# Performance work log

Measured on AMD Instinct MI355X. Metric: run time of the kernel, lower is better.

The kernel has to match this reference:

```python
import jax, jax.numpy as jnp
import numpy as np

MARGIN = 0.1  # GatingFunction margin_threshold default


def _gating(x, gW1, gb1, gW2, gb2):
    # two-layer MLP + softmax over experts: [B, E]
    h = jax.nn.relu(x @ gW1 + gb1)
    probs = jax.nn.softmax(h @ gW2 + gb2, axis=1)

    # sequential per-sample running-assignment masking (training + mask_enabled path)
    def step(rta, s):
        rta1 = rta + s
        mask = rta1 > rta1.mean() + MARGIN
        rta2 = jnp.where(mask.any(), rta1 - s, rta1)  # subtract back only if any masked
        mod = jnp.where(mask, 0.0, s)
        norm = mod.sum()
        mod = mod / jnp.where(norm == 0, 1.0, norm)
        return rta2 + mod, mod

    rta0 = jnp.zeros((gW2.shape[1],), probs.dtype)  # running_total_assignment buffer
    _, gate = jax.lax.scan(step, rta0, probs)
    # torch code writes detached modified samples into modified_x -> no grad through gate
    return jax.lax.stop_gradient(gate)


def reference(x_expert, gW1, gb1, gW2, gb2, eW1, eb1, eW2, eb2):
    gate = _gating(x_expert, gW1, gb1, gW2, gb2)          # [B, E]
    # all experts run densely: [B, E, H] -> [B, E, O]
    h = jax.nn.relu(jnp.einsum('bi,eih->beh', x_expert, eW1) + eb1)
    expert_out = jnp.einsum('beh,eho->beo', h, eW2) + eb2
    g = gate[:, :, None]                                   # [B, E, 1]
    # fallback if every gate value is zero (torch's all-zero check)
    g = jnp.where(jnp.all(g == 0), jnp.ones_like(g) / g.shape[1], g)
    output = jnp.sum(g * expert_out, axis=1)               # [B, O]
    return output, g


def setup_inputs() -> dict:
    B, IN, HID, OUT, E = 4096, 1024, 4096, 1024, 8
    key = jax.random.key(0)
    ks = jax.random.split(key, 9)
    s = 0.02
    return {
        'x_expert': jax.random.normal(ks[0], (B, IN), jnp.float32),
        'gW1': jax.random.normal(ks[1], (IN, HID), jnp.float32) * s,
        'gb1': jnp.zeros((HID,), jnp.float32),
        'gW2': jax.random.normal(ks[2], (HID, E), jnp.float32) * s,
        'gb2': jnp.zeros((E,), jnp.float32),
        'eW1': jax.random.normal(ks[3], (E, IN, HID), jnp.float32) * s,
        'eb1': jnp.zeros((E, HID), jnp.float32),
        'eW2': jax.random.normal(ks[4], (E, HID, OUT), jnp.float32) * s,
        'eb2': jnp.zeros((E, OUT), jnp.float32),
    }
```

## Files before the change

kernel.cpp:

```cpp
#include <hip/hip_runtime.h>
#include <stdint.h>

using f32x4  = __attribute__((ext_vector_type(4))) float;
using bf16x8 = __attribute__((ext_vector_type(8))) __bf16;

static __device__ __forceinline__ unsigned short f2bf(float f) {
  union { float f; unsigned int u; } v; v.f = f;
  return (unsigned short)((v.u + 0x7fffu + ((v.u >> 16) & 1u)) >> 16);
}

static __device__ __forceinline__ void gload_lds16(const void* g, void* l) {
  __builtin_amdgcn_global_load_lds((const __attribute__((address_space(1))) void*)g,
                                   (__attribute__((address_space(3))) void*)l,
                                   16, 0, 0);
}

static __device__ __forceinline__ int swz(int row) { return (row & 3) ^ ((row >> 2) & 3); }

template <int CTRL>
static __device__ __forceinline__ float dppadd(float x) {
  int xi = __builtin_bit_cast(int, x);
  int yi = __builtin_amdgcn_update_dpp(0, xi, CTRL, 0xF, 0xF, true);
  return x + __builtin_bit_cast(float, yi);
}
static __device__ __forceinline__ float redsum8(float x) {
  float t = dppadd<0xB1>(x);
  t = dppadd<0x4E>(t);
  t = dppadd<0x124>(t);
  return t;
}

__global__ __launch_bounds__(256) void k_cvt_bf16(const float* __restrict__ in,
                                                  unsigned short* __restrict__ out) {
  int i = blockIdx.x * 256 + threadIdx.x;
  float4 v = ((const float4*)in)[i];
  ushort4 o;
  o.x = f2bf(v.x); o.y = f2bf(v.y); o.z = f2bf(v.z); o.w = f2bf(v.w);
  ((ushort4*)out)[i] = o;
}

__global__ __launch_bounds__(256) void k_transpose_cvt(const float* __restrict__ in,
                                                       unsigned short* __restrict__ out,
                                                       int R, int C) {
  __shared__ float tile[32][33];
  int e = blockIdx.z;
  const float* ip = in + (size_t)e * R * C;
  unsigned short* op = out + (size_t)e * R * C;
  int c0 = blockIdx.x * 32, r0 = blockIdx.y * 32;
  int tx = threadIdx.x, ty = threadIdx.y;
  #pragma unroll
  for (int i = ty; i < 32; i += 8)
    tile[i][tx] = ip[(size_t)(r0 + i) * C + c0 + tx];
  __syncthreads();
  #pragma unroll
  for (int i = ty; i < 32; i += 8)
    op[(size_t)(c0 + i) * R + r0 + tx] = f2bf(tile[tx][i]);
}

__global__ __launch_bounds__(256) void k_gemm_f32_relu(const float* __restrict__ A,
                                                       const float* __restrict__ Bm,
                                                       const float* __restrict__ bias,
                                                       float* __restrict__ C) {
  const int K = 1024, N = 4096;
  __shared__ float As[16][128];
  __shared__ float Bs[16][128];
  int n0 = blockIdx.x * 128, m0 = blockIdx.y * 128;
  int t = threadIdx.x;
  int tm = t >> 4, tn = t & 15;
  float acc[8][8];
  #pragma unroll
  for (int i = 0; i < 8; ++i)
    #pragma unroll
    for (int j = 0; j < 8; ++j) acc[i][j] = 0.f;

  for (int k0 = 0; k0 < K; k0 += 16) {
    __syncthreads();
    #pragma unroll
    for (int cc = 0; cc < 2; ++cc) {
      int c = t + cc * 256;
      int m = c >> 2, kq = c & 3;
      float4 v = *(const float4*)&A[(size_t)(m0 + m) * K + k0 + kq * 4];
      As[kq * 4 + 0][m] = v.x; As[kq * 4 + 1][m] = v.y;
      As[kq * 4 + 2][m] = v.z; As[kq * 4 + 3][m] = v.w;
    }
    #pragma unroll
    for (int cc = 0; cc < 2; ++cc) {
      int c = t + cc * 256;
      int kr = c >> 5, nq = c & 31;
      *(float4*)&Bs[kr][nq * 4] = *(const float4*)&Bm[(size_t)(k0 + kr) * N + n0 + nq * 4];
    }
    __syncthreads();
    #pragma unroll
    for (int kk = 0; kk < 16; ++kk) {
      float a[8], b[8];
      *(float4*)&a[0] = *(const float4*)&As[kk][tm * 8];
      *(float4*)&a[4] = *(const float4*)&As[kk][tm * 8 + 4];
      *(float4*)&b[0] = *(const float4*)&Bs[kk][tn * 8];
      *(float4*)&b[4] = *(const float4*)&Bs[kk][tn * 8 + 4];
      #pragma unroll
      for (int i = 0; i < 8; ++i)
        #pragma unroll
        for (int j = 0; j < 8; ++j) acc[i][j] = fmaf(a[i], b[j], acc[i][j]);
    }
  }
  float bb[8];
  #pragma unroll
  for (int j = 0; j < 8; ++j) bb[j] = bias[n0 + tn * 8 + j];
  #pragma unroll
  for (int i = 0; i < 8; ++i) {
    int m = m0 + tm * 8 + i;
    float* crow = C + (size_t)m * N + n0 + tn * 8;
    float4 v0, v1;
    v0.x = fmaxf(acc[i][0] + bb[0], 0.f); v0.y = fmaxf(acc[i][1] + bb[1], 0.f);
    v0.z = fmaxf(acc[i][2] + bb[2], 0.f); v0.w = fmaxf(acc[i][3] + bb[3], 0.f);
    v1.x = fmaxf(acc[i][4] + bb[4], 0.f); v1.y = fmaxf(acc[i][5] + bb[5], 0.f);
    v1.z = fmaxf(acc[i][6] + bb[6], 0.f); v1.w = fmaxf(acc[i][7] + bb[7], 0.f);
    *(float4*)crow = v0; *(float4*)(crow + 4) = v1;
  }
}

__global__ __launch_bounds__(256) void k_gate2_softmax(const float* __restrict__ Hg,
                                                       const float* __restrict__ gW2,
                                                       const float* __restrict__ gb2,
                                                       float* __restrict__ probs) {
  __shared__ float red[4][8];
  int b = blockIdx.x, t = threadIdx.x;
  const float* hrow = Hg + (size_t)b * 4096;
  float acc[8];
  #pragma unroll
  for (int e = 0; e < 8; ++e) acc[e] = 0.f;
  #pragma unroll
  for (int i = 0; i < 4; ++i) {
    int kk = t + i * 256;
    float4 h = ((const float4*)hrow)[kk];
    const float* wr = gW2 + (size_t)kk * 32;
    #pragma unroll
    for (int j = 0; j < 4; ++j) {
      float hv = (&h.x)[j];
      #pragma unroll
      for (int e = 0; e < 8; ++e) acc[e] = fmaf(hv, wr[j * 8 + e], acc[e]);
    }
  }
  #pragma unroll
  for (int e = 0; e < 8; ++e) {
    float v = acc[e];
    for (int off = 32; off > 0; off >>= 1) v += __shfl_down(v, off);
    acc[e] = v;
  }
  int lane = t & 63, w = t >> 6;
  if (lane == 0) {
    #pragma unroll
    for (int e = 0; e < 8; ++e) red[w][e] = acc[e];
  }
  __syncthreads();
  if (t == 0) {
    float l[8], mx = -1e30f;
    #pragma unroll
    for (int e = 0; e < 8; ++e) {
      l[e] = red[0][e] + red[1][e] + red[2][e] + red[3][e] + gb2[e];
      mx = fmaxf(mx, l[e]);
    }
    float sum = 0.f;
    #pragma unroll
    for (int e = 0; e < 8; ++e) { l[e] = expf(l[e] - mx); sum += l[e]; }
    float inv = 1.f / sum;
    #pragma unroll
    for (int e = 0; e < 8; ++e) probs[b * 8 + e] = l[e] * inv;
  }
}

__global__ __launch_bounds__(256) void k_egemm1_scan(const unsigned short* __restrict__ Xb,
                                                     const unsigned short* __restrict__ W1T,
                                                     const float* __restrict__ eb1,
                                                     const float* __restrict__ probs,
                                                     float* __restrict__ gateOut,
                                                     unsigned short* __restrict__ Hs) {
  __shared__ __align__(16) char smem[33024];
  int bid = blockIdx.x;
  int t = threadIdx.x;

  if (bid == 0) {
    float* P  = (float*)smem;
    float* G  = P + 4096;
    int*  flg = (int*)(G + 4096);
    int e = t & 7;
    float rta = 0.f, maxn = 0.f;
    for (int ch = 0; ch < 8; ++ch) {
      __syncthreads();
      #pragma unroll
      for (int i = 0; i < 4; ++i)
        ((float4*)P)[t + i * 256] = ((const float4*)(probs + ch * 4096))[t + i * 256];
      __syncthreads();
      if (t < 64) {
        float s_cur = P[e];
        for (int r = 0; r < 512; ++r) {
          float s_nxt = P[(((r + 1) & 511) << 3) + e];
          float a = rta + s_cur;
          float sum = redsum8(a);
          float thr = fmaf(sum, 0.125f, 0.1f);
          bool msk = a > thr;
          unsigned long long bal = __ballot(msk);
          float d = msk ? 0.f : s_cur;
          float norm = redsum8(d);
          float inv = (norm == 0.f) ? 1.f : (1.f / norm);
          float g = d * inv;
          float base = (bal != 0ull) ? (a - s_cur) : a;
          rta = base + g;
          maxn = fmaxf(maxn, norm);
          if (t < 8) G[(r << 3) + e] = g;
          s_cur = s_nxt;
        }
      }
      __syncthreads();
      #pragma unroll
      for (int i = 0; i < 4; ++i)
        ((float4*)(gateOut + ch * 4096))[t + i * 256] = ((const float4*)G)[t + i * 256];
    }
    if (t == 0) *flg = (maxn > 0.f) ? 1 : 0;
    __syncthreads();
    if (*flg == 0) {
      for (int i = t; i < 32768; i += 256) gateOut[i] = 0.125f;
    }
    return;
  }

  char* Asm = smem;
  char* Bsm = smem + 8192;
  int b = bid - 1;
  int e = b >> 10;
  int rest = b & 1023;
  int m0 = (rest >> 5) << 7, n0 = (rest & 31) << 7;
  int lane = t & 63, w = t >> 6;
  int wm = w >> 1, wn = w & 1;
  const unsigned short* Ab = Xb;
  const unsigned short* Bb = W1T + ((size_t)e << 22);
  f32x4 acc[4][4];
  #pragma unroll
  for (int mi = 0; mi < 4; ++mi)
    #pragma unroll
    for (int ni = 0; ni < 4; ++ni) acc[mi][ni] = (f32x4){0.f, 0.f, 0.f, 0.f};

  for (int kt = 0; kt < 1024; kt += 32) {
    __syncthreads();
    {
      int p = (w << 6) + lane;
      int row = p >> 2, h = (p & 3) ^ swz(row);
      int p2 = p + 256;
      int row2 = p2 >> 2, h2 = (p2 & 3) ^ swz(row2);
      char* la = Asm + (w << 10);
      char* lb = Bsm + (w << 10);
      gload_lds16(Ab + (size_t)(m0 + row) * 1024 + kt + h * 8, la);
      gload_lds16(Ab + (size_t)(m0 + row2) * 1024 + kt + h2 * 8, la + 4096);
      gload_lds16(Bb + (size_t)(n0 + row) * 1024 + kt + h * 8, lb);
      gload_lds16(Bb + (size_t)(n0 + row2) * 1024 + kt + h2 * 8, lb + 4096);
    }
    __syncthreads();
    bf16x8 af[4], bfr[4];
    #pragma unroll
    for (int mi = 0; mi < 4; ++mi) {
      int ra = (wm << 6) + (mi << 4) + (lane & 15);
      int hh = (lane >> 4) ^ swz(ra);
      af[mi] = *(const bf16x8*)(Asm + ra * 64 + hh * 16);
    }
    #pragma unroll
    for (int ni = 0; ni < 4; ++ni) {
      int rb = (wn << 6) + (ni << 4) + (lane & 15);
      int hh = (lane >> 4) ^ swz(rb);
      bfr[ni] = *(const bf16x8*)(Bsm + rb * 64 + hh * 16);
    }
    #pragma unroll
    for (int mi = 0; mi < 4; ++mi)
      #pragma unroll
      for (int ni = 0; ni < 4; ++ni)
        acc[mi][ni] = __builtin_amdgcn_mfma_f32_16x16x32_bf16(af[mi], bfr[ni], acc[mi][ni], 0, 0, 0);
  }
  const float* b1e = eb1 + (e << 12);
  unsigned short* Ho = Hs + ((size_t)e << 24);
  int col = lane & 15, quad = lane >> 4;
  float bn[4];
  #pragma unroll
  for (int ni = 0; ni < 4; ++ni) bn[ni] = b1e[n0 + (wn << 6) + (ni << 4) + col];
  #pragma unroll
  for (int mi = 0; mi < 4; ++mi) {
    #pragma unroll
    for (int r = 0; r < 4; ++r) {
      int m = m0 + (wm << 6) + (mi << 4) + (quad << 2) + r;
      unsigned short* orow = Ho + (size_t)m * 4096 + n0 + (wn << 6) + col;
      #pragma unroll
      for (int ni = 0; ni < 4; ++ni) {
        float v = fmaxf(acc[mi][ni][r] + bn[ni], 0.f);
        orow[ni << 4] = f2bf(v);
      }
    }
  }
}

__global__ __launch_bounds__(256) void k_egemm2(const unsigned short* __restrict__ Hs,
                                                const unsigned short* __restrict__ W2T,
                                                float* __restrict__ partLo,
                                                float* __restrict__ partHi) {
  __shared__ __align__(16) char Asm[8192];
  __shared__ __align__(16) char Bsm[8192];
  int bid = blockIdx.x;
  int n0 = (bid >> 8) << 7;
  int rem = bid & 255;
  int m0 = (rem >> 3) << 7;
  int e = rem & 7;
  int t = threadIdx.x, lane = t & 63, w = t >> 6;
  int wm = w >> 1, wn = w & 1;
  const unsigned short* Ab = Hs + ((size_t)e << 24);
  const unsigned short* Bb = W2T + ((size_t)e << 22);
  f32x4 acc[4][4];
  #pragma unroll
  for (int mi = 0; mi < 4; ++mi)
    #pragma unroll
    for (int ni = 0; ni < 4; ++ni) acc[mi][ni] = (f32x4){0.f, 0.f, 0.f, 0.f};

  for (int kt = 0; kt < 4096; kt += 32) {
    __syncthreads();
    {
      int p = (w << 6) + lane;
      int row = p >> 2, h = (p & 3) ^ swz(row);
      int p2 = p + 256;
      int row2 = p2 >> 2, h2 = (p2 & 3) ^ swz(row2);
      char* la = Asm + (w << 10);
      char* lb = Bsm + (w << 10);
      gload_lds16(Ab + (size_t)(m0 + row) * 4096 + kt + h * 8, la);
      gload_lds16(Ab + (size_t)(m0 + row2) * 4096 + kt + h2 * 8, la + 4096);
      gload_lds16(Bb + (size_t)(n0 + row) * 4096 + kt + h * 8, lb);
      gload_lds16(Bb + (size_t)(n0 + row2) * 4096 + kt + h2 * 8, lb + 4096);
    }
    __syncthreads();
    bf16x8 af[4], bfr[4];
    #pragma unroll
    for (int mi = 0; mi < 4; ++mi) {
      int ra = (wm << 6) + (mi << 4) + (lane & 15);
      int hh = (lane >> 4) ^ swz(ra);
      af[mi] = *(const bf16x8*)(Asm + ra * 64 + hh * 16);
    }
    #pragma unroll
    for (int ni = 0; ni < 4; ++ni) {
      int rb = (wn << 6) + (ni << 4) + (lane & 15);
      int hh = (lane >> 4) ^ swz(rb);
      bfr[ni] = *(const bf16x8*)(Bsm + rb * 64 + hh * 16);
    }
    #pragma unroll
    for (int mi = 0; mi < 4; ++mi)
      #pragma unroll
      for (int ni = 0; ni < 4; ++ni)
        acc[mi][ni] = __builtin_amdgcn_mfma_f32_16x16x32_bf16(af[mi], bfr[ni], acc[mi][ni], 0, 0, 0);
  }
  float* Pe = (e < 4 ? partLo + ((size_t)e << 22) : partHi + ((size_t)(e - 4) << 22));
  int col = lane & 15, quad = lane >> 4;
  #pragma unroll
  for (int mi = 0; mi < 4; ++mi) {
    #pragma unroll
    for (int r = 0; r < 4; ++r) {
      int m = m0 + (wm << 6) + (mi << 4) + (quad << 2) + r;
      float* orow = Pe + (size_t)m * 1024 + n0 + (wn << 6) + col;
      #pragma unroll
      for (int ni = 0; ni < 4; ++ni) orow[ni << 4] = acc[mi][ni][r];
    }
  }
}

__global__ __launch_bounds__(256) void k_reduce(const float* __restrict__ partLo,
                                                const float* __restrict__ partHi,
                                                const float* __restrict__ eb2,
                                                const float* __restrict__ gate,
                                                float* __restrict__ Out) {
  int idx = blockIdx.x * 256 + threadIdx.x;
  int m = idx >> 8, n4 = idx & 255;
  float4 g0 = *(const float4*)(gate + (m << 3));
  float4 g1 = *(const float4*)(gate + (m << 3) + 4);
  float ga[8] = {g0.x, g0.y, g0.z, g0.w, g1.x, g1.y, g1.z, g1.w};
  float4 acc = make_float4(0.f, 0.f, 0.f, 0.f);
  #pragma unroll
  for (int e = 0; e < 8; ++e) {
    const float* Pe = (e < 4 ? partLo + ((size_t)e << 22) : partHi + ((size_t)(e - 4) << 22));
    float4 pv = ((const float4*)Pe)[idx];
    float4 bv = ((const float4*)(eb2 + (e << 10)))[n4];
    acc.x += ga[e] * (pv.x + bv.x);
    acc.y += ga[e] * (pv.y + bv.y);
    acc.z += ga[e] * (pv.z + bv.z);
    acc.w += ga[e] * (pv.w + bv.w);
  }
  ((float4*)Out)[idx] = acc;
}

extern "C" void kernel_launch(void* const* d_in, const int* in_sizes, int n_in,
                              void* d_out, int out_size, void* d_ws, size_t ws_size,
                              hipStream_t stream) {
  (void)in_sizes; (void)n_in; (void)out_size; (void)ws_size;
  const float* x   = (const float*)d_in[0];
  const float* gW1 = (const float*)d_in[1];
  const float* gb1 = (const float*)d_in[2];
  const float* gW2 = (const float*)d_in[3];
  const float* gb2 = (const float*)d_in[4];
  const float* eW1 = (const float*)d_in[5];
  const float* eb1 = (const float*)d_in[6];
  const float* eW2 = (const float*)d_in[7];
  const float* eb2 = (const float*)d_in[8];
  float* out = (float*)d_out;
  float* gateOut = out + (size_t)4096 * 1024;

  char* ws = (char*)d_ws;
  unsigned short* Xb  = (unsigned short*)ws;
  unsigned short* W1T = (unsigned short*)(ws + (8ull  << 20));
  unsigned short* W2T = (unsigned short*)(ws + (72ull << 20));
  float*          prb = (float*)        (ws + (136ull << 20));
  float*          Hg  = (float*)        (ws + (137ull << 20));
  unsigned short* Hs  = (unsigned short*)(ws + (201ull << 20));
  float* partLo = (float*)(ws + (8ull   << 20));
  float* partHi = (float*)(ws + (137ull << 20));

  k_cvt_bf16<<<4096, 256, 0, stream>>>(x, Xb);
  k_transpose_cvt<<<dim3(128, 32, 8), dim3(32, 8), 0, stream>>>(eW1, W1T, 1024, 4096);
  k_transpose_cvt<<<dim3(32, 128, 8), dim3(32, 8), 0, stream>>>(eW2, W2T, 4096, 1024);
  k_gemm_f32_relu<<<dim3(32, 32), 256, 0, stream>>>(x, gW1, gb1, Hg);
  k_gate2_softmax<<<4096, 256, 0, stream>>>(Hg, gW2, gb2, prb);
  k_egemm1_scan<<<8193, 256, 0, stream>>>(Xb, W1T, eb1, prb, gateOut, Hs);
  k_egemm2<<<2048, 256, 0, stream>>>(Hs, W2T, partLo, partHi);
  k_reduce<<<4096, 256, 0, stream>>>(partLo, partHi, eb2, gateOut, out);
}
```

Baseline: 1.894 ms.

## Enlarge gating GEMM tile, transpose MFMA operands for vectorized epilogue stores, shrink scan LDS

```diff
diff --git a/kernel.cpp b/kernel.cpp
--- a/kernel.cpp
+++ b/kernel.cpp
@@ -4,9 +4,12 @@
 using f32x4  = __attribute__((ext_vector_type(4))) float;
 using bf16x8 = __attribute__((ext_vector_type(8))) __bf16;
 
+static __device__ __forceinline__ unsigned int f2bf_u(float f) {
+  union { float f; unsigned int u; } v; v.f = f;
+  return (v.u + 0x7fffu + ((v.u >> 16) & 1u)) >> 16;
+}
 static __device__ __forceinline__ unsigned short f2bf(float f) {
-  union { float f; unsigned int u; } v; v.f = f;
-  return (unsigned short)((v.u + 0x7fffu + ((v.u >> 16) & 1u)) >> 16);
+  return (unsigned short)f2bf_u(f);
 }
 
 static __device__ __forceinline__ void gload_lds16(const void* g, void* l) {
@@ -57,26 +60,26 @@
     op[(size_t)(c0 + i) * R + r0 + tx] = f2bf(tile[tx][i]);
 }
 
-__global__ __launch_bounds__(256) void k_gemm_f32_relu(const float* __restrict__ A,
-                                                       const float* __restrict__ Bm,
-                                                       const float* __restrict__ bias,
-                                                       float* __restrict__ C) {
+__global__ __launch_bounds__(256, 2) void k_gemm_f32_relu(const float* __restrict__ A,
+                                                          const float* __restrict__ Bm,
+                                                          const float* __restrict__ bias,
+                                                          float* __restrict__ C) {
   const int K = 1024, N = 4096;
-  __shared__ float As[16][128];
+  __shared__ float As[16][256];
   __shared__ float Bs[16][128];
-  int n0 = blockIdx.x * 128, m0 = blockIdx.y * 128;
+  int n0 = blockIdx.x * 128, m0 = blockIdx.y * 256;
   int t = threadIdx.x;
   int tm = t >> 4, tn = t & 15;
-  float acc[8][8];
-  #pragma unroll
-  for (int i = 0; i < 8; ++i)
+  float acc[16][8];
+  #pragma unroll
+  for (int i = 0; i < 16; ++i)
     #pragma unroll
     for (int j = 0; j < 8; ++j) acc[i][j] = 0.f;
 
   for (int k0 = 0; k0 < K; k0 += 16) {
     __syncthreads();
     #pragma unroll
-    for (int cc = 0; cc < 2; ++cc) {
+    for (int cc = 0; cc < 4; ++cc) {
       int c = t + cc * 256;
       int m = c >> 2, kq = c & 3;
       float4 v = *(const float4*)&A[(size_t)(m0 + m) * K + k0 + kq * 4];
@@ -92,13 +95,14 @@
     __syncthreads();
     #pragma unroll
     for (int kk = 0; kk < 16; ++kk) {
-      float a[8], b[8];
-      *(float4*)&a[0] = *(const float4*)&As[kk][tm * 8];
-      *(float4*)&a[4] = *(const float4*)&As[kk][tm * 8 + 4];
+      float a[16], b[8];
+      #pragma unroll
+      for (int q = 0; q < 4; ++q)
+        *(float4*)&a[q * 4] = *(const float4*)&As[kk][tm * 16 + q * 4];
       *(float4*)&b[0] = *(const float4*)&Bs[kk][tn * 8];
       *(float4*)&b[4] = *(const float4*)&Bs[kk][tn * 8 + 4];
       #pragma unroll
-      for (int i = 0; i < 8; ++i)
+      for (int i = 0; i < 16; ++i)
         #pragma unroll
         for (int j = 0; j < 8; ++j) acc[i][j] = fmaf(a[i], b[j], acc[i][j]);
     }
@@ -107,8 +111,8 @@
   #pragma unroll
   for (int j = 0; j < 8; ++j) bb[j] = bias[n0 + tn * 8 + j];
   #pragma unroll
-  for (int i = 0; i < 8; ++i) {
-    int m = m0 + tm * 8 + i;
+  for (int i = 0; i < 16; ++i) {
+    int m = m0 + tm * 16 + i;
     float* crow = C + (size_t)m * N + n0 + tn * 8;
     float4 v0, v1;
     v0.x = fmaxf(acc[i][0] + bb[0], 0.f); v0.y = fmaxf(acc[i][1] + bb[1], 0.f);
@@ -175,26 +179,26 @@
                                                      const float* __restrict__ probs,
                                                      float* __restrict__ gateOut,
                                                      unsigned short* __restrict__ Hs) {
-  __shared__ __align__(16) char smem[33024];
+  __shared__ __align__(16) char smem[16512];
   int bid = blockIdx.x;
   int t = threadIdx.x;
 
   if (bid == 0) {
     float* P  = (float*)smem;
-    float* G  = P + 4096;
-    int*  flg = (int*)(G + 4096);
+    float* G  = P + 2048;
+    int*  flg = (int*)(G + 2048);
     int e = t & 7;
     float rta = 0.f, maxn = 0.f;
-    for (int ch = 0; ch < 8; ++ch) {
+    for (int ch = 0; ch < 16; ++ch) {
       __syncthreads();
       #pragma unroll
-      for (int i = 0; i < 4; ++i)
-        ((float4*)P)[t + i * 256] = ((const float4*)(probs + ch * 4096))[t + i * 256];
+      for (int i = 0; i < 2; ++i)
+        ((float4*)P)[t + i * 256] = ((const float4*)(probs + ch * 2048))[t + i * 256];
       __syncthreads();
       if (t < 64) {
         float s_cur = P[e];
-        for (int r = 0; r < 512; ++r) {
-          float s_nxt = P[(((r + 1) & 511) << 3) + e];
+        for (int r = 0; r < 256; ++r) {
+          float s_nxt = P[(((r + 1) & 255) << 3) + e];
           float a = rta + s_cur;
           float sum = redsum8(a);
           float thr = fmaf(sum, 0.125f, 0.1f);
@@ -213,8 +217,8 @@
       }
       __syncthreads();
       #pragma unroll
-      for (int i = 0; i < 4; ++i)
-        ((float4*)(gateOut + ch * 4096))[t + i * 256] = ((const float4*)G)[t + i * 256];
+      for (int i = 0; i < 2; ++i)
+        ((float4*)(gateOut + ch * 2048))[t + i * 256] = ((const float4*)G)[t + i * 256];
     }
     if (t == 0) *flg = (maxn > 0.f) ? 1 : 0;
     __syncthreads();
@@ -272,25 +276,29 @@
     for (int mi = 0; mi < 4; ++mi)
       #pragma unroll
       for (int ni = 0; ni < 4; ++ni)
-        acc[mi][ni] = __builtin_amdgcn_mfma_f32_16x16x32_bf16(af[mi], bfr[ni], acc[mi][ni], 0, 0, 0);
+        acc[mi][ni] = __builtin_amdgcn_mfma_f32_16x16x32_bf16(bfr[ni], af[mi], acc[mi][ni], 0, 0, 0);
   }
   const float* b1e = eb1 + (e << 12);
   unsigned short* Ho = Hs + ((size_t)e << 24);
   int col = lane & 15, quad = lane >> 4;
-  float bn[4];
-  #pragma unroll
-  for (int ni = 0; ni < 4; ++ni) bn[ni] = b1e[n0 + (wn << 6) + (ni << 4) + col];
+  float4 bq[4];
+  #pragma unroll
+  for (int ni = 0; ni < 4; ++ni)
+    bq[ni] = *(const float4*)&b1e[n0 + (wn << 6) + (ni << 4) + (quad << 2)];
   #pragma unroll
   for (int mi = 0; mi < 4; ++mi) {
-    #pragma unroll
-    for (int r = 0; r < 4; ++r) {
-      int m = m0 + (wm << 6) + (mi << 4) + (quad << 2) + r;
-      unsigned short* orow = Ho + (size_t)m * 4096 + n0 + (wn << 6) + col;
-      #pragma unroll
-      for (int ni = 0; ni < 4; ++ni) {
-        float v = fmaxf(acc[mi][ni][r] + bn[ni], 0.f);
-        orow[ni << 4] = f2bf(v);
-      }
+    int m = m0 + (wm << 6) + (mi << 4) + col;
+    unsigned short* orow = Ho + (size_t)m * 4096 + n0 + (wn << 6) + (quad << 2);
+    #pragma unroll
+    for (int ni = 0; ni < 4; ++ni) {
+      float v0 = fmaxf(acc[mi][ni][0] + bq[ni].x, 0.f);
+      float v1 = fmaxf(acc[mi][ni][1] + bq[ni].y, 0.f);
+      float v2 = fmaxf(acc[mi][ni][2] + bq[ni].z, 0.f);
+      float v3 = fmaxf(acc[mi][ni][3] + bq[ni].w, 0.f);
+      uint2 u;
+      u.x = f2bf_u(v0) | (f2bf_u(v1) << 16);
+      u.y = f2bf_u(v2) | (f2bf_u(v3) << 16);
+      *(uint2*)(orow + (ni << 4)) = u;
     }
   }
 }
@@ -348,18 +356,20 @@
     for (int mi = 0; mi < 4; ++mi)
       #pragma unroll
       for (int ni = 0; ni < 4; ++ni)
-        acc[mi][ni] = __builtin_amdgcn_mfma_f32_16x16x32_bf16(af[mi], bfr[ni], acc[mi][ni], 0, 0, 0);
+        acc[mi][ni] = __builtin_amdgcn_mfma_f32_16x16x32_bf16(bfr[ni], af[mi], acc[mi][ni], 0, 0, 0);
   }
   float* Pe = (e < 4 ? partLo + ((size_t)e << 22) : partHi + ((size_t)(e - 4) << 22));
   int col = lane & 15, quad = lane >> 4;
   #pragma unroll
   for (int mi = 0; mi < 4; ++mi) {
-    #pragma unroll
-    for (int r = 0; r < 4; ++r) {
-      int m = m0 + (wm << 6) + (mi << 4) + (quad << 2) + r;
-      float* orow = Pe + (size_t)m * 1024 + n0 + (wn << 6) + col;
-      #pragma unroll
-      for (int ni = 0; ni < 4; ++ni) orow[ni << 4] = acc[mi][ni][r];
+    int m = m0 + (wm << 6) + (mi << 4) + col;
+    float* orow = Pe + (size_t)m * 1024 + n0 + (wn << 6) + (quad << 2);
+    #pragma unroll
+    for (int ni = 0; ni < 4; ++ni) {
+      float4 v;
+      v.x = acc[mi][ni][0]; v.y = acc[mi][ni][1];
+      v.z = acc[mi][ni][2]; v.w = acc[mi][ni][3];
+      *(float4*)(orow + (ni << 4)) = v;
     }
   }
 }
@@ -417,7 +427,7 @@
   k_cvt_bf16<<<4096, 256, 0, stream>>>(x, Xb);
   k_transpose_cvt<<<dim3(128, 32, 8), dim3(32, 8), 0, stream>>>(eW1, W1T, 1024, 4096);
   k_transpose_cvt<<<dim3(32, 128, 8), dim3(32, 8), 0, stream>>>(eW2, W2T, 4096, 1024);
-  k_gemm_f32_relu<<<dim3(32, 32), 256, 0, stream>>>(x, gW1, gb1, Hg);
+  k_gemm_f32_relu<<<dim3(32, 16), 256, 0, stream>>>(x, gW1, gb1, Hg);
   k_gate2_softmax<<<4096, 256, 0, stream>>>(Hg, gW2, gb2, prb);
   k_egemm1_scan<<<8193, 256, 0, stream>>>(Xb, W1T, eb1, prb, gateOut, Hs);
   k_egemm2<<<2048, 256, 0, stream>>>(Hs, W2T, partLo, partHi);
```

New measurement: 1.912 ms. No clear change (+0.9%).
